# Performance work log

Hardware: AMD Instinct MI355X
Metric: run time of the kernel (lower is better)

The kernel has to match this reference:

```python
import jax, jax.numpy as jnp
import numpy as np

N_NODES = 100000
N_EDGES = 1600000
D = 128          # in_dim == out_dim
H = 8            # num_heads
DH = D // H      # head dim = 16
DFF = 2 * D
EPS_LN = 1e-5


def _ln(x, g, b):
    mu = jnp.mean(x, axis=-1, keepdims=True)
    var = jnp.var(x, axis=-1, keepdims=True)
    return (x - mu) * jax.lax.rsqrt(var + EPS_LN) * g + b


def setup_inputs() -> dict:
    key = jax.random.key(0)
    ks = jax.random.split(key, 12)
    s = 1.0 / np.sqrt(D)
    inp = {
        "h": jax.random.normal(ks[0], (N_NODES, D), jnp.float32),
        "src": jax.random.randint(ks[1], (N_EDGES,), 0, N_NODES, jnp.int32),
        "dst": jax.random.randint(ks[2], (N_EDGES,), 0, N_NODES, jnp.int32),
        "Wq": jax.random.normal(ks[3], (D, D), jnp.float32) * s,
        "Wk": jax.random.normal(ks[4], (D, D), jnp.float32) * s,
        "Wv": jax.random.normal(ks[5], (D, D), jnp.float32) * s,
        "Wo": jax.random.normal(ks[6], (D, D), jnp.float32) * s,
        "bo": jnp.zeros((D,), jnp.float32),
        "ln1_g": jnp.ones((D,), jnp.float32),
        "ln1_b": jnp.zeros((D,), jnp.float32),
        "W1": jax.random.normal(ks[7], (D, DFF), jnp.float32) * s,
        "b1": jnp.zeros((DFF,), jnp.float32),
        "W2": jax.random.normal(ks[8], (DFF, D), jnp.float32) * (1.0 / np.sqrt(DFF)),
        "b2": jnp.zeros((D,), jnp.float32),
        "ln2_g": jnp.ones((D,), jnp.float32),
        "ln2_b": jnp.zeros((D,), jnp.float32),
    }
    return inp


def reference(h, src, dst, Wq, Wk, Wv, Wo, bo, ln1_g, ln1_b, W1, b1, W2, b2, ln2_g, ln2_b):
    n = h.shape[0]
    # Q/K/V projections (no bias), split into heads: [N, H, DH]
    Q = (h @ Wq).reshape(n, H, DH)
    K = (h @ Wk).reshape(n, H, DH)
    V = (h @ Wv).reshape(n, H, DH)

    # edge-wise attention score: K[src] . Q[dst] / sqrt(DH), exp-clamped
    score = jnp.einsum("ehd,ehd->eh", K[src], Q[dst]) / np.sqrt(DH)  # [E, H]
    score = jnp.exp(jnp.clip(score, -5.0, 5.0))

    # weighted message sum + normalizer via segment reduce over dst
    m = V[src] * score[:, :, None]                                   # [E, H, DH]
    wV = jax.ops.segment_sum(m, dst, num_segments=n)                 # [N, H, DH]
    z = jax.ops.segment_sum(score, dst, num_segments=n)              # [N, H]

    h_attn = (wV / (z[:, :, None] + 1e-6)).reshape(n, D)

    # output projection + residual + LN
    x = h + (h_attn @ Wo + bo)
    x = _ln(x, ln1_g, ln1_b)

    # FFN + residual + LN
    y = jax.nn.relu(x @ W1 + b1) @ W2 + b2
    x = _ln(x + y, ln2_g, ln2_b)
    return x
```

## Files before the change

### kernel.cpp

```cpp
#include <hip/hip_runtime.h>
#include <hip/hip_bf16.h>
#include <math.h>


typedef __attribute__((ext_vector_type(8))) short bf16x8;
typedef __attribute__((ext_vector_type(4))) float f32x4;
typedef __attribute__((ext_vector_type(2))) _Float16 half2_t;

#define BSHIFT 9
#define BSIZE  512

static __device__ __forceinline__ half2_t h2(unsigned u) {
    return __builtin_bit_cast(half2_t, u);
}
static __device__ __forceinline__ float bl(unsigned u) {
    return __uint_as_float(u << 16);
}
static __device__ __forceinline__ float bh(unsigned u) {
    return __uint_as_float(u & 0xffff0000u);
}

template<int K, bool AF32, bool RELU, bool LN, bool RESID, bool BIAS, bool YW, bool F16O>
__global__ __launch_bounds__(256)
void gemm_mfma(const void* __restrict__ Ap, int lda,
               const __hip_bfloat16* __restrict__ Bt, int ldbt,
               const float* __restrict__ bias, const float* __restrict__ resid,
               const float* __restrict__ lng, const float* __restrict__ lnb,
               float* __restrict__ Cf, __hip_bfloat16* __restrict__ Cb, int ldc,
               size_t bt_ystride, size_t cb_ystride, int N)
{
    constexpr int CK = 128;
    __shared__ unsigned short As[64 * 136];
    __shared__ unsigned short Bs[128 * 136];

    const int tid  = threadIdx.x;
    const int row0 = blockIdx.x * 64;
    int col0 = 0;
    if (YW) { Bt += blockIdx.y * bt_ystride; Cb += blockIdx.y * cb_ystride; }
    else    col0 = blockIdx.y * 128;

    const int wave = tid >> 6, lane = tid & 63;
    const int quad = lane >> 4, l15 = lane & 15;

    f32x4 acc[8];
    #pragma unroll
    for (int t = 0; t < 8; ++t) acc[t] = (f32x4)0.f;

    for (int kc = 0; kc < K; kc += CK) {
        #pragma unroll
        for (int it = 0; it < 4; ++it) {
            int i = tid + it * 256;
            int r = i >> 4, kb = i & 15;
            int rg = row0 + r; if (rg > N - 1) rg = N - 1;
            if (AF32) {
                const float* Af = (const float*)Ap;
                const float4 f0 = *(const float4*)&Af[(size_t)rg * lda + kc + kb * 8];
                const float4 f1 = *(const float4*)&Af[(size_t)rg * lda + kc + kb * 8 + 4];
                __hip_bfloat162 b01 = __float22bfloat162_rn(make_float2(f0.x, f0.y));
                __hip_bfloat162 b23 = __float22bfloat162_rn(make_float2(f0.z, f0.w));
                __hip_bfloat162 b45 = __float22bfloat162_rn(make_float2(f1.x, f1.y));
                __hip_bfloat162 b67 = __float22bfloat162_rn(make_float2(f1.z, f1.w));
                uint4 u;
                u.x = *(unsigned*)&b01; u.y = *(unsigned*)&b23;
                u.z = *(unsigned*)&b45; u.w = *(unsigned*)&b67;
                *(uint4*)&As[r * 136 + kb * 8] = u;
            } else {
                const __hip_bfloat16* Ab = (const __hip_bfloat16*)Ap;
                *(uint4*)&As[r * 136 + kb * 8] =
                    *(const uint4*)&Ab[(size_t)rg * lda + kc + kb * 8];
            }
        }
        #pragma unroll
        for (int it = 0; it < 8; ++it) {
            int i = tid + it * 256;
            int r = i >> 4, kb = i & 15;
            *(uint4*)&Bs[r * 136 + kb * 8] =
                *(const uint4*)&Bt[(size_t)(col0 + r) * ldbt + kc + kb * 8];
        }
        __syncthreads();
        const unsigned short* ap = &As[(wave * 16 + l15) * 136 + quad * 8];
        const unsigned short* bp = &Bs[l15 * 136 + quad * 8];
        #pragma unroll
        for (int ks = 0; ks < 4; ++ks) {
            bf16x8 a = *(const bf16x8*)(ap + ks * 32);
            #pragma unroll
            for (int t = 0; t < 8; ++t) {
                bf16x8 b = *(const bf16x8*)(bp + t * 16 * 136 + ks * 32);
                acc[t] = __builtin_amdgcn_mfma_f32_16x16x32_bf16(a, b, acc[t], 0, 0, 0);
            }
        }
        __syncthreads();
    }

    const int rbase = row0 + wave * 16 + quad * 4;

    float vals[8][4];
    #pragma unroll
    for (int t = 0; t < 8; ++t) {
        float bv = BIAS ? bias[col0 + t * 16 + l15] : 0.f;
        #pragma unroll
        for (int i = 0; i < 4; ++i) vals[t][i] = acc[t][i] + bv;
    }
    if (RESID) {
        #pragma unroll
        for (int i = 0; i < 4; ++i) {
            int row = rbase + i;
            if (row < N) {
                #pragma unroll
                for (int t = 0; t < 8; ++t)
                    vals[t][i] += resid[(size_t)row * 128 + t * 16 + l15];
            }
        }
    }
    if (RELU) {
        #pragma unroll
        for (int t = 0; t < 8; ++t)
            #pragma unroll
            for (int i = 0; i < 4; ++i) vals[t][i] = fmaxf(vals[t][i], 0.f);
    }
    if (LN) {
        #pragma unroll
        for (int i = 0; i < 4; ++i) {
            float s = 0.f, sq = 0.f;
            #pragma unroll
            for (int t = 0; t < 8; ++t) { float v = vals[t][i]; s += v; sq += v * v; }
            s  += __shfl_xor(s, 1);  s  += __shfl_xor(s, 2);
            s  += __shfl_xor(s, 4);  s  += __shfl_xor(s, 8);
            sq += __shfl_xor(sq, 1); sq += __shfl_xor(sq, 2);
            sq += __shfl_xor(sq, 4); sq += __shfl_xor(sq, 8);
            float m  = s * (1.f / 128.f);
            float rs = rsqrtf(sq * (1.f / 128.f) - m * m + 1e-5f);
            #pragma unroll
            for (int t = 0; t < 8; ++t) {
                float g = lng[t * 16 + l15], b = lnb[t * 16 + l15];
                vals[t][i] = (vals[t][i] - m) * rs * g + b;
            }
        }
    }
    #pragma unroll
    for (int i = 0; i < 4; ++i) {
        int row = rbase + i;
        if (row >= N) continue;
        if (Cf) {
            #pragma unroll
            for (int t = 0; t < 8; ++t)
                Cf[(size_t)row * ldc + col0 + t * 16 + l15] = vals[t][i];
        }
        if (Cb) {
            #pragma unroll
            for (int t = 0; t < 8; ++t) {
                if (F16O)
                    ((_Float16*)Cb)[(size_t)row * ldc + col0 + t * 16 + l15] =
                        (_Float16)vals[t][i];
                else
                    Cb[(size_t)row * ldc + col0 + t * 16 + l15] =
                        __float2bfloat16(vals[t][i]);
            }
        }
    }
}

struct WArgs {
    const float* src[6];
    __hip_bfloat16* dst[6];
    int R[6], C[6];
};
__global__ __launch_bounds__(256)
void cast_w(WArgs wa)
{
    int w = blockIdx.y;
    int R = wa.R[w], C = wa.C[w];
    int i = blockIdx.x * 256 + threadIdx.x;
    if (i >= R * C) return;
    int sh = (C == 256) ? 8 : 7;
    int r = i >> sh, c = i & (C - 1);
    wa.dst[w][(size_t)c * R + r] = __float2bfloat16(wa.src[w][i]);
}

__global__ __launch_bounds__(256)
void bucket_hist(const int* __restrict__ dst, int* __restrict__ bCnt,
                 int E, int chunk, int NB)
{
    __shared__ int bh[256];
    const int t = threadIdx.x;
    bh[t] = 0;
    __syncthreads();
    const int s0 = blockIdx.x * chunk;
    const int s1 = min(E, s0 + chunk);
    for (int i = s0 + t; i < s1; i += 256)
        atomicAdd(&bh[dst[i] >> BSHIFT], 1);
    __syncthreads();
    if (t < NB && bh[t]) atomicAdd(&bCnt[t], bh[t]);
}

__global__ __launch_bounds__(256)
void bucket_scan(const int* __restrict__ bCnt, int* __restrict__ bBase,
                 int* __restrict__ gCur, int* __restrict__ rowStart,
                 int N, int E, int NB)
{
    __shared__ int wsum[4];
    const int t = threadIdx.x, lane = t & 63, wv = t >> 6;
    int v = (t < NB) ? bCnt[t] : 0;
    const int s = v;
    for (int off = 1; off < 64; off <<= 1) {
        int u = __shfl_up(v, off);
        if (lane >= off) v += u;
    }
    if (lane == 63) wsum[wv] = v;
    __syncthreads();
    int add = 0;
    for (int w = 0; w < wv; ++w) add += wsum[w];
    const int excl = v + add - s;
    if (t <= NB) bBase[t] = excl;
    if (t < NB)  gCur[t]  = excl;
    if (t == 0)  rowStart[N] = E;
}

__global__ __launch_bounds__(256)
void partition_kernel(const int* __restrict__ src, const int* __restrict__ dst,
                      int* __restrict__ gCur, uint2* __restrict__ P,
                      int E, int chunk, int NB)
{
    __shared__ int ch[256];
    __shared__ int cur[256];
    const int t = threadIdx.x;
    ch[t] = 0;
    __syncthreads();
    const int s0 = blockIdx.x * chunk;
    const int s1 = min(E, s0 + chunk);
    for (int i = s0 + t; i < s1; i += 256)
        atomicAdd(&ch[dst[i] >> BSHIFT], 1);
    __syncthreads();
    if (t < NB) {
        int c = ch[t];
        cur[t] = c ? atomicAdd(&gCur[t], c) : 0;
    }
    __syncthreads();
    for (int i = s0 + t; i < s1; i += 256) {
        int d = dst[i];
        int pos = atomicAdd(&cur[d >> BSHIFT], 1);
        P[pos] = make_uint2((unsigned)src[i], (unsigned)d);
    }
}

__global__ __launch_bounds__(256)
void bucket_scatter(const uint2* __restrict__ P, const int* __restrict__ bBase,
                    int* __restrict__ rowStart, int* __restrict__ esrc, int N)
{
    __shared__ int hist[BSIZE];
    __shared__ int cur[BSIZE];
    __shared__ int wsum[4];

    const int b  = blockIdx.x;
    const int t  = threadIdx.x;
    const int d0 = b << BSHIFT;
    const int bb  = bBase[b];
    const int cnt = bBase[b + 1] - bb;

    hist[t] = 0; hist[t + 256] = 0;
    __syncthreads();
    for (int i = t; i < cnt; i += 256)
        atomicAdd(&hist[(int)P[bb + i].y - d0], 1);
    __syncthreads();

    {
        const int a0 = hist[2 * t], a1 = hist[2 * t + 1];
        int v = a0 + a1;
        const int s = v;
        const int lane = t & 63, wv = t >> 6;
        for (int off = 1; off < 64; off <<= 1) {
            int u = __shfl_up(v, off);
            if (lane >= off) v += u;
        }
        if (lane == 63) wsum[wv] = v;
        __syncthreads();
        int add = 0;
        for (int w = 0; w < wv; ++w) add += wsum[w];
        const int exclT = v + add - s;
        cur[2 * t]     = exclT;
        cur[2 * t + 1] = exclT + a0;
    }
    __syncthreads();
    for (int i = t; i < BSIZE; i += 256) {
        int d = d0 + i;
        if (d < N) rowStart[d] = bb + cur[i];
    }
    __syncthreads();
    for (int i = t; i < cnt; i += 256) {
        uint2 p = P[bb + i];
        int pos = atomicAdd(&cur[(int)p.y - d0], 1);
        esrc[bb + pos] = (int)p.x;
    }
}

__global__ __launch_bounds__(256)
void aggregate_kernel(unsigned short* __restrict__ Qp,
                      const unsigned short* __restrict__ KV,
                      const int* __restrict__ esrc,
                      const int* __restrict__ rowStart, int N)
{
    const int lane = threadIdx.x & 63;
    const int wid  = threadIdx.x >> 6;
    const int d    = blockIdx.x * 4 + wid;
    if (d >= N) return;

    const int c = lane & 15;
    const int g = lane >> 4;

    const uint4 qraw = *(const uint4*)(Qp + (size_t)d * 128u + c * 8);
    const half2_t q0 = h2(qraw.x), q1 = h2(qraw.y),
                  q2 = h2(qraw.z), q3 = h2(qraw.w);

    const int beg = rowStart[d];
    const int end = rowStart[d + 1];

    float a0 = 0.f, a1 = 0.f, a2 = 0.f, a3 = 0.f;
    float a4 = 0.f, a5 = 0.f, a6 = 0.f, a7 = 0.f, z = 0.f;
    const float S = 0.36067376022224085f;
    const float C = 7.2134752044448170f;
    const char* KVb = (const char*)KV + (size_t)c * 16;

    for (int base = beg; base < end; base += 64) {
        int n = end - base; if (n > 64) n = 64;
        const int mysrc = (lane < n) ? esrc[base + lane] : 0;
        const int jmax = (n + 3) >> 2;
        #pragma unroll 2
        for (int j = 0; j < jmax; ++j) {
            const int idx = j * 4 + g;
            const bool valid = idx < n;
            const int s = __shfl(mysrc, valid ? idx : n - 1);
            const char* bp = KVb + (size_t)(unsigned)s * 512u;
            const uint4 kr = *(const uint4*)bp;
            const uint4 vr = *(const uint4*)(bp + 256);
            float p = __builtin_amdgcn_fdot2(h2(kr.x), q0, 0.f, false);
            p = __builtin_amdgcn_fdot2(h2(kr.y), q1, p, false);
            p = __builtin_amdgcn_fdot2(h2(kr.z), q2, p, false);
            p = __builtin_amdgcn_fdot2(h2(kr.w), q3, p, false);
            p += __shfl_xor(p, 1);
            float se = exp2f(fminf(C, fmaxf(-C, p * S)));
            se = valid ? se : 0.f;
            a0 += bl(vr.x) * se; a1 += bh(vr.x) * se;
            a2 += bl(vr.y) * se; a3 += bh(vr.y) * se;
            a4 += bl(vr.z) * se; a5 += bh(vr.z) * se;
            a6 += bl(vr.w) * se; a7 += bh(vr.w) * se;
            z  += se;
        }
    }

    a0 += __shfl_xor(a0, 16); a1 += __shfl_xor(a1, 16);
    a2 += __shfl_xor(a2, 16); a3 += __shfl_xor(a3, 16);
    a4 += __shfl_xor(a4, 16); a5 += __shfl_xor(a5, 16);
    a6 += __shfl_xor(a6, 16); a7 += __shfl_xor(a7, 16);
    z  += __shfl_xor(z, 16);
    a0 += __shfl_xor(a0, 32); a1 += __shfl_xor(a1, 32);
    a2 += __shfl_xor(a2, 32); a3 += __shfl_xor(a3, 32);
    a4 += __shfl_xor(a4, 32); a5 += __shfl_xor(a5, 32);
    a6 += __shfl_xor(a6, 32); a7 += __shfl_xor(a7, 32);
    z  += __shfl_xor(z, 32);

    if (g == 0) {
        const float inv = 1.0f / (z + 1e-6f);
        __hip_bfloat162 p0 = __float22bfloat162_rn(make_float2(a0 * inv, a1 * inv));
        __hip_bfloat162 p1 = __float22bfloat162_rn(make_float2(a2 * inv, a3 * inv));
        __hip_bfloat162 p2 = __float22bfloat162_rn(make_float2(a4 * inv, a5 * inv));
        __hip_bfloat162 p3 = __float22bfloat162_rn(make_float2(a6 * inv, a7 * inv));
        uint4 o;
        o.x = *(unsigned*)&p0; o.y = *(unsigned*)&p1;
        o.z = *(unsigned*)&p2; o.w = *(unsigned*)&p3;
        *(uint4*)(Qp + (size_t)d * 128u + c * 8) = o;
    }
}

extern "C" void kernel_launch(void* const* d_in, const int* in_sizes, int n_in,
                              void* d_out, int out_size, void* d_ws, size_t ws_size,
                              hipStream_t stream)
{
    const float* h    = (const float*)d_in[0];
    const int*   src  = (const int*)  d_in[1];
    const int*   dst  = (const int*)  d_in[2];
    const float* Wq   = (const float*)d_in[3];
    const float* Wk   = (const float*)d_in[4];
    const float* Wv   = (const float*)d_in[5];
    const float* Wo   = (const float*)d_in[6];
    const float* bo   = (const float*)d_in[7];
    const float* ln1g = (const float*)d_in[8];
    const float* ln1b = (const float*)d_in[9];
    const float* W1   = (const float*)d_in[10];
    const float* b1   = (const float*)d_in[11];
    const float* W2   = (const float*)d_in[12];
    const float* b2   = (const float*)d_in[13];
    const float* ln2g = (const float*)d_in[14];
    const float* ln2b = (const float*)d_in[15];

    const int N = in_sizes[0] / 128;
    const int E = in_sizes[1];
    const int NB = (N + BSIZE - 1) >> BSHIFT;

    unsigned short* Qh = (unsigned short*)d_ws;
    unsigned short* KV = Qh + (size_t)N * 128;
    __hip_bfloat16* Xh = (__hip_bfloat16*)(KV + (size_t)N * 256);
    float*          Xf = (float*)(Xh + (size_t)N * 128);
    __hip_bfloat16* Wt = (__hip_bfloat16*)(Xf + (size_t)N * 128);
    __hip_bfloat16* Wqt = Wt;
    __hip_bfloat16* Wkt = Wqt + 16384;
    __hip_bfloat16* Wvt = Wkt + 16384;
    __hip_bfloat16* Wot = Wvt + 16384;
    __hip_bfloat16* W1t = Wot + 16384;
    __hip_bfloat16* W2t = W1t + 32768;
    int* ib       = (int*)(W2t + 32768);
    int* bCnt     = ib;
    int* bBase    = ib + 256;
    int* gCur     = ib + 514;
    int* rowStart = ib + 770;
    int* esrc     = ib + 770 + N + 2;
    uint2* P      = (uint2*)Xf;
    __hip_bfloat16* Th = (__hip_bfloat16*)KV;

    const dim3 blk(256);
    const int  nb    = (N + 63) / 64;
    const int  chunk = (E + 255) / 256;

    WArgs wa;
    wa.src[0] = Wq; wa.src[1] = Wk; wa.src[2] = Wv; wa.src[3] = Wo; wa.src[4] = W1; wa.src[5] = W2;
    wa.dst[0] = Wqt; wa.dst[1] = Wkt; wa.dst[2] = Wvt; wa.dst[3] = Wot; wa.dst[4] = W1t; wa.dst[5] = W2t;
    wa.R[0] = wa.R[1] = wa.R[2] = wa.R[3] = 128; wa.R[4] = 128; wa.R[5] = 256;
    wa.C[0] = wa.C[1] = wa.C[2] = wa.C[3] = 128; wa.C[4] = 256; wa.C[5] = 128;
    cast_w<<<dim3(128, 6), blk, 0, stream>>>(wa);

    gemm_mfma<128,true,false,false,false,false,false,true><<<dim3(nb, 1), blk, 0, stream>>>(
        h, 128, Wqt, 128, nullptr, nullptr, nullptr, nullptr,
        nullptr, (__hip_bfloat16*)Qh, 128, 0, 0, N);
    gemm_mfma<128,true,false,false,false,false,false,true><<<dim3(nb, 1), blk, 0, stream>>>(
        h, 128, Wkt, 128, nullptr, nullptr, nullptr, nullptr,
        nullptr, (__hip_bfloat16*)KV, 256, 0, 0, N);
    gemm_mfma<128,true,false,false,false,false,false,false><<<dim3(nb, 1), blk, 0, stream>>>(
        h, 128, Wvt, 128, nullptr, nullptr, nullptr, nullptr,
        nullptr, (__hip_bfloat16*)(KV + 128), 256, 0, 0, N);

    hipMemsetAsync(bCnt, 0, 256 * sizeof(int), stream);
    bucket_hist<<<dim3(256), blk, 0, stream>>>(dst, bCnt, E, chunk, NB);
    bucket_scan<<<dim3(1), blk, 0, stream>>>(bCnt, bBase, gCur, rowStart, N, E, NB);
    partition_kernel<<<dim3(256), blk, 0, stream>>>(src, dst, gCur, P, E, chunk, NB);
    bucket_scatter<<<dim3(NB), blk, 0, stream>>>(P, bBase, rowStart, esrc, N);

    aggregate_kernel<<<dim3((N + 3) / 4), blk, 0, stream>>>(Qh, KV, esrc, rowStart, N);

    gemm_mfma<128,false,false,true,true,true,false,false><<<dim3(nb, 1), blk, 0, stream>>>(
        (__hip_bfloat16*)Qh, 128, Wot, 128, bo, h, ln1g, ln1b, Xf, Xh, 128, 0, 0, N);

    gemm_mfma<128,false,true,false,false,true,false,false><<<dim3(nb, 2), blk, 0, stream>>>(
        Xh, 128, W1t, 128, b1, nullptr, nullptr, nullptr, nullptr, Th, 256, 0, 0, N);

    gemm_mfma<256,false,false,true,true,true,false,false><<<dim3(nb, 1), blk, 0, stream>>>(
        Th, 256, W2t, 256, b2, Xf, ln2g, ln2b, (float*)d_out, nullptr, 128, 0, 0, N);
}
```

Measured before the change: 431.8 us.

## Fuse Q/K/V projections into one kernel and loop W1 column halves in-block

Replaces three separate Q, K and V GEMM launches with one kernel that converts each 64-row tile of h to bf16 once and reuses it for all three weight matrices. The W1 GEMM now loops over both 128-column halves inside a block instead of using a 2-wide grid, so the A tile is loaded once. The bucket counter memset is folded into the weight-cast kernel. The aim is to cut repeated reads of h and Xh and to remove launch overhead. In exchange, each block does more serial work with fewer blocks in flight.

Result: faster. 419.9 us (-2.8%).

```diff
diff --git a/kernel.cpp b/kernel.cpp
--- a/kernel.cpp
+++ b/kernel.cpp
@@ -20,139 +20,205 @@
     return __uint_as_float(u & 0xffff0000u);
 }
 
-template<int K, bool AF32, bool RELU, bool LN, bool RESID, bool BIAS, bool YW, bool F16O>
-__global__ __launch_bounds__(256)
-void gemm_mfma(const void* __restrict__ Ap, int lda,
+__global__ __launch_bounds__(256)
+void qkv_fused(const float* __restrict__ h,
+               const __hip_bfloat16* __restrict__ Wqt,
+               const __hip_bfloat16* __restrict__ Wkt,
+               const __hip_bfloat16* __restrict__ Wvt,
+               unsigned short* __restrict__ Qh,
+               unsigned short* __restrict__ KV,
+               int N)
+{
+    __shared__ unsigned short As[64 * 136];
+    __shared__ unsigned short Bs[128 * 136];
+
+    const int tid  = threadIdx.x;
+    const int row0 = blockIdx.x * 64;
+    const int wave = tid >> 6, lane = tid & 63;
+    const int quad = lane >> 4, l15 = lane & 15;
+
+    #pragma unroll
+    for (int it = 0; it < 4; ++it) {
+        int i = tid + it * 256;
+        int r = i >> 4, kb = i & 15;
+        int rg = row0 + r; if (rg > N - 1) rg = N - 1;
+        const float4 f0 = *(const float4*)&h[(size_t)rg * 128 + kb * 8];
+        const float4 f1 = *(const float4*)&h[(size_t)rg * 128 + kb * 8 + 4];
+        __hip_bfloat162 b01 = __float22bfloat162_rn(make_float2(f0.x, f0.y));
+        __hip_bfloat162 b23 = __float22bfloat162_rn(make_float2(f0.z, f0.w));
+        __hip_bfloat162 b45 = __float22bfloat162_rn(make_float2(f1.x, f1.y));
+        __hip_bfloat162 b67 = __float22bfloat162_rn(make_float2(f1.z, f1.w));
+        uint4 u;
+        u.x = *(unsigned*)&b01; u.y = *(unsigned*)&b23;
+        u.z = *(unsigned*)&b45; u.w = *(unsigned*)&b67;
+        *(uint4*)&As[r * 136 + kb * 8] = u;
+    }
+
+    const __hip_bfloat16* Ws[3] = { Wqt, Wkt, Wvt };
+
+    #pragma unroll
+    for (int w = 0; w < 3; ++w) {
+        #pragma unroll
+        for (int it = 0; it < 8; ++it) {
+            int i = tid + it * 256;
+            int r = i >> 4, kb = i & 15;
+            *(uint4*)&Bs[r * 136 + kb * 8] =
+                *(const uint4*)&Ws[w][(size_t)r * 128 + kb * 8];
+        }
+        __syncthreads();
+
+        f32x4 acc[8];
+        #pragma unroll
+        for (int t = 0; t < 8; ++t) acc[t] = (f32x4)0.f;
+
+        const unsigned short* ap = &As[(wave * 16 + l15) * 136 + quad * 8];
+        const unsigned short* bp = &Bs[l15 * 136 + quad * 8];
+        #pragma unroll
+        for (int ks = 0; ks < 4; ++ks) {
+            bf16x8 a = *(const bf16x8*)(ap + ks * 32);
+            #pragma unroll
+            for (int t = 0; t < 8; ++t) {
+                bf16x8 b = *(const bf16x8*)(bp + t * 16 * 136 + ks * 32);
+                acc[t] = __builtin_amdgcn_mfma_f32_16x16x32_bf16(a, b, acc[t], 0, 0, 0);
+            }
+        }
+        __syncthreads();
+
+        const int rbase = row0 + wave * 16 + quad * 4;
+        #pragma unroll
+        for (int i = 0; i < 4; ++i) {
+            int row = rbase + i;
+            if (row >= N) continue;
+            #pragma unroll
+            for (int t = 0; t < 8; ++t) {
+                float v = acc[t][i];
+                if (w == 0)
+                    ((_Float16*)Qh)[(size_t)row * 128 + t * 16 + l15] = (_Float16)v;
+                else if (w == 1)
+                    ((_Float16*)KV)[(size_t)row * 256 + t * 16 + l15] = (_Float16)v;
+                else
+                    ((__hip_bfloat16*)KV)[(size_t)row * 256 + 128 + t * 16 + l15] =
+                        __float2bfloat16(v);
+            }
+        }
+    }
+}
+
+template<int K, int YLOOP, bool RELU, bool LN, bool RESID, bool BIAS>
+__global__ __launch_bounds__(256)
+void gemm_mfma(const __hip_bfloat16* __restrict__ Ab, int lda,
                const __hip_bfloat16* __restrict__ Bt, int ldbt,
                const float* __restrict__ bias, const float* __restrict__ resid,
                const float* __restrict__ lng, const float* __restrict__ lnb,
                float* __restrict__ Cf, __hip_bfloat16* __restrict__ Cb, int ldc,
-               size_t bt_ystride, size_t cb_ystride, int N)
+               int N)
 {
     constexpr int CK = 128;
+    static_assert(YLOOP == 1 || K == CK, "YLOOP>1 needs single K chunk");
     __shared__ unsigned short As[64 * 136];
     __shared__ unsigned short Bs[128 * 136];
 
     const int tid  = threadIdx.x;
     const int row0 = blockIdx.x * 64;
-    int col0 = 0;
-    if (YW) { Bt += blockIdx.y * bt_ystride; Cb += blockIdx.y * cb_ystride; }
-    else    col0 = blockIdx.y * 128;
-
     const int wave = tid >> 6, lane = tid & 63;
     const int quad = lane >> 4, l15 = lane & 15;
-
-    f32x4 acc[8];
-    #pragma unroll
-    for (int t = 0; t < 8; ++t) acc[t] = (f32x4)0.f;
-
-    for (int kc = 0; kc < K; kc += CK) {
-        #pragma unroll
-        for (int it = 0; it < 4; ++it) {
-            int i = tid + it * 256;
-            int r = i >> 4, kb = i & 15;
-            int rg = row0 + r; if (rg > N - 1) rg = N - 1;
-            if (AF32) {
-                const float* Af = (const float*)Ap;
-                const float4 f0 = *(const float4*)&Af[(size_t)rg * lda + kc + kb * 8];
-                const float4 f1 = *(const float4*)&Af[(size_t)rg * lda + kc + kb * 8 + 4];
-                __hip_bfloat162 b01 = __float22bfloat162_rn(make_float2(f0.x, f0.y));
-                __hip_bfloat162 b23 = __float22bfloat162_rn(make_float2(f0.z, f0.w));
-                __hip_bfloat162 b45 = __float22bfloat162_rn(make_float2(f1.x, f1.y));
-                __hip_bfloat162 b67 = __float22bfloat162_rn(make_float2(f1.z, f1.w));
-                uint4 u;
-                u.x = *(unsigned*)&b01; u.y = *(unsigned*)&b23;
-                u.z = *(unsigned*)&b45; u.w = *(unsigned*)&b67;
-                *(uint4*)&As[r * 136 + kb * 8] = u;
-            } else {
-                const __hip_bfloat16* Ab = (const __hip_bfloat16*)Ap;
-                *(uint4*)&As[r * 136 + kb * 8] =
-                    *(const uint4*)&Ab[(size_t)rg * lda + kc + kb * 8];
-            }
-        }
-        #pragma unroll
-        for (int it = 0; it < 8; ++it) {
-            int i = tid + it * 256;
-            int r = i >> 4, kb = i & 15;
-            *(uint4*)&Bs[r * 136 + kb * 8] =
-                *(const uint4*)&Bt[(size_t)(col0 + r) * ldbt + kc + kb * 8];
-        }
-        __syncthreads();
-        const unsigned short* ap = &As[(wave * 16 + l15) * 136 + quad * 8];
-        const unsigned short* bp = &Bs[l15 * 136 + quad * 8];
-        #pragma unroll
-        for (int ks = 0; ks < 4; ++ks) {
-            bf16x8 a = *(const bf16x8*)(ap + ks * 32);
-            #pragma unroll
-            for (int t = 0; t < 8; ++t) {
-                bf16x8 b = *(const bf16x8*)(bp + t * 16 * 136 + ks * 32);
-                acc[t] = __builtin_amdgcn_mfma_f32_16x16x32_bf16(a, b, acc[t], 0, 0, 0);
-            }
-        }
-        __syncthreads();
-    }
-
     const int rbase = row0 + wave * 16 + quad * 4;
 
-    float vals[8][4];
-    #pragma unroll
-    for (int t = 0; t < 8; ++t) {
-        float bv = BIAS ? bias[col0 + t * 16 + l15] : 0.f;
-        #pragma unroll
-        for (int i = 0; i < 4; ++i) vals[t][i] = acc[t][i] + bv;
-    }
-    if (RESID) {
+    for (int yy = 0; yy < YLOOP; ++yy) {
+        const int col0 = yy * 128;
+
+        f32x4 acc[8];
+        #pragma unroll
+        for (int t = 0; t < 8; ++t) acc[t] = (f32x4)0.f;
+
+        for (int kc = 0; kc < K; kc += CK) {
+            if (yy == 0) {
+                #pragma unroll
+                for (int it = 0; it < 4; ++it) {
+                    int i = tid + it * 256;
+                    int r = i >> 4, kb = i & 15;
+                    int rg = row0 + r; if (rg > N - 1) rg = N - 1;
+                    *(uint4*)&As[r * 136 + kb * 8] =
+                        *(const uint4*)&Ab[(size_t)rg * lda + kc + kb * 8];
+                }
+            }
+            #pragma unroll
+            for (int it = 0; it < 8; ++it) {
+                int i = tid + it * 256;
+                int r = i >> 4, kb = i & 15;
+                *(uint4*)&Bs[r * 136 + kb * 8] =
+                    *(const uint4*)&Bt[(size_t)(col0 + r) * ldbt + kc + kb * 8];
+            }
+            __syncthreads();
+            const unsigned short* ap = &As[(wave * 16 + l15) * 136 + quad * 8];
+            const unsigned short* bp = &Bs[l15 * 136 + quad * 8];
+            #pragma unroll
+            for (int ks = 0; ks < 4; ++ks) {
+                bf16x8 a = *(const bf16x8*)(ap + ks * 32);
+                #pragma unroll
+                for (int t = 0; t < 8; ++t) {
+                    bf16x8 b = *(const bf16x8*)(bp + t * 16 * 136 + ks * 32);
+                    acc[t] = __builtin_amdgcn_mfma_f32_16x16x32_bf16(a, b, acc[t], 0, 0, 0);
+                }
+            }
+            __syncthreads();
+        }
+
+        float vals[8][4];
+        #pragma unroll
+        for (int t = 0; t < 8; ++t) {
+            float bv = BIAS ? bias[col0 + t * 16 + l15] : 0.f;
+            #pragma unroll
+            for (int i = 0; i < 4; ++i) vals[t][i] = acc[t][i] + bv;
+        }
+        if (RESID) {
+            #pragma unroll
+            for (int i = 0; i < 4; ++i) {
+                int row = rbase + i;
+                if (row < N) {
+                    #pragma unroll
+                    for (int t = 0; t < 8; ++t)
+                        vals[t][i] += resid[(size_t)row * 128 + t * 16 + l15];
+                }
+            }
+        }
+        if (RELU) {
+            #pragma unroll
+            for (int t = 0; t < 8; ++t)
+                #pragma unroll
+                for (int i = 0; i < 4; ++i) vals[t][i] = fmaxf(vals[t][i], 0.f);
+        }
+        if (LN) {
+            #pragma unroll
+            for (int i = 0; i < 4; ++i) {
+                float s = 0.f, sq = 0.f;
+                #pragma unroll
+                for (int t = 0; t < 8; ++t) { float v = vals[t][i]; s += v; sq += v * v; }
+                s  += __shfl_xor(s, 1);  s  += __shfl_xor(s, 2);
+                s  += __shfl_xor(s, 4);  s  += __shfl_xor(s, 8);
+                sq += __shfl_xor(sq, 1); sq += __shfl_xor(sq, 2);
+                sq += __shfl_xor(sq, 4); sq += __shfl_xor(sq, 8);
+                float m  = s * (1.f / 128.f);
+                float rs = rsqrtf(sq * (1.f / 128.f) - m * m + 1e-5f);
+                #pragma unroll
+                for (int t = 0; t < 8; ++t) {
+                    float g = lng[t * 16 + l15], b = lnb[t * 16 + l15];
+                    vals[t][i] = (vals[t][i] - m) * rs * g + b;
+                }
+            }
+        }
         #pragma unroll
         for (int i = 0; i < 4; ++i) {
             int row = rbase + i;
-            if (row < N) {
+            if (row >= N) continue;
+            if (Cf) {
                 #pragma unroll
                 for (int t = 0; t < 8; ++t)
-                    vals[t][i] += resid[(size_t)row * 128 + t * 16 + l15];
-            }
-        }
-    }
-    if (RELU) {
-        #pragma unroll
-        for (int t = 0; t < 8; ++t)
-            #pragma unroll
-            for (int i = 0; i < 4; ++i) vals[t][i] = fmaxf(vals[t][i], 0.f);
-    }
-    if (LN) {
-        #pragma unroll
-        for (int i = 0; i < 4; ++i) {
-            float s = 0.f, sq = 0.f;
-            #pragma unroll
-            for (int t = 0; t < 8; ++t) { float v = vals[t][i]; s += v; sq += v * v; }
-            s  += __shfl_xor(s, 1);  s  += __shfl_xor(s, 2);
-            s  += __shfl_xor(s, 4);  s  += __shfl_xor(s, 8);
-            sq += __shfl_xor(sq, 1); sq += __shfl_xor(sq, 2);
-            sq += __shfl_xor(sq, 4); sq += __shfl_xor(sq, 8);
-            float m  = s * (1.f / 128.f);
-            float rs = rsqrtf(sq * (1.f / 128.f) - m * m + 1e-5f);
-            #pragma unroll
-            for (int t = 0; t < 8; ++t) {
-                float g = lng[t * 16 + l15], b = lnb[t * 16 + l15];
-                vals[t][i] = (vals[t][i] - m) * rs * g + b;
-            }
-        }
-    }
-    #pragma unroll
-    for (int i = 0; i < 4; ++i) {
-        int row = rbase + i;
-        if (row >= N) continue;
-        if (Cf) {
-            #pragma unroll
-            for (int t = 0; t < 8; ++t)
-                Cf[(size_t)row * ldc + col0 + t * 16 + l15] = vals[t][i];
-        }
-        if (Cb) {
-            #pragma unroll
-            for (int t = 0; t < 8; ++t) {
-                if (F16O)
-                    ((_Float16*)Cb)[(size_t)row * ldc + col0 + t * 16 + l15] =
-                        (_Float16)vals[t][i];
-                else
+                    Cf[(size_t)row * ldc + col0 + t * 16 + l15] = vals[t][i];
+            }
+            if (Cb) {
+                #pragma unroll
+                for (int t = 0; t < 8; ++t)
                     Cb[(size_t)row * ldc + col0 + t * 16 + l15] =
                         __float2bfloat16(vals[t][i]);
             }
@@ -166,8 +232,9 @@
     int R[6], C[6];
 };
 __global__ __launch_bounds__(256)
-void cast_w(WArgs wa)
-{
+void cast_w(WArgs wa, int* __restrict__ bCnt)
+{
+    if (blockIdx.x == 0 && blockIdx.y == 0) bCnt[threadIdx.x] = 0;
     int w = blockIdx.y;
     int R = wa.R[w], C = wa.C[w];
     int i = blockIdx.x * 256 + threadIdx.x;
@@ -425,19 +492,10 @@
     wa.dst[0] = Wqt; wa.dst[1] = Wkt; wa.dst[2] = Wvt; wa.dst[3] = Wot; wa.dst[4] = W1t; wa.dst[5] = W2t;
     wa.R[0] = wa.R[1] = wa.R[2] = wa.R[3] = 128; wa.R[4] = 128; wa.R[5] = 256;
     wa.C[0] = wa.C[1] = wa.C[2] = wa.C[3] = 128; wa.C[4] = 256; wa.C[5] = 128;
-    cast_w<<<dim3(128, 6), blk, 0, stream>>>(wa);
-
-    gemm_mfma<128,true,false,false,false,false,false,true><<<dim3(nb, 1), blk, 0, stream>>>(
-        h, 128, Wqt, 128, nullptr, nullptr, nullptr, nullptr,
-        nullptr, (__hip_bfloat16*)Qh, 128, 0, 0, N);
-    gemm_mfma<128,true,false,false,false,false,false,true><<<dim3(nb, 1), blk, 0, stream>>>(
-        h, 128, Wkt, 128, nullptr, nullptr, nullptr, nullptr,
-        nullptr, (__hip_bfloat16*)KV, 256, 0, 0, N);
-    gemm_mfma<128,true,false,false,false,false,false,false><<<dim3(nb, 1), blk, 0, stream>>>(
-        h, 128, Wvt, 128, nullptr, nullptr, nullptr, nullptr,
-        nullptr, (__hip_bfloat16*)(KV + 128), 256, 0, 0, N);
-
-    hipMemsetAsync(bCnt, 0, 256 * sizeof(int), stream);
+    cast_w<<<dim3(128, 6), blk, 0, stream>>>(wa, bCnt);
+
+    qkv_fused<<<dim3(nb), blk, 0, stream>>>(h, Wqt, Wkt, Wvt, Qh, KV, N);
+
     bucket_hist<<<dim3(256), blk, 0, stream>>>(dst, bCnt, E, chunk, NB);
     bucket_scan<<<dim3(1), blk, 0, stream>>>(bCnt, bBase, gCur, rowStart, N, E, NB);
     partition_kernel<<<dim3(256), blk, 0, stream>>>(src, dst, gCur, P, E, chunk, NB);
@@ -445,12 +503,12 @@
 
     aggregate_kernel<<<dim3((N + 3) / 4), blk, 0, stream>>>(Qh, KV, esrc, rowStart, N);
 
-    gemm_mfma<128,false,false,true,true,true,false,false><<<dim3(nb, 1), blk, 0, stream>>>(
-        (__hip_bfloat16*)Qh, 128, Wot, 128, bo, h, ln1g, ln1b, Xf, Xh, 128, 0, 0, N);
-
-    gemm_mfma<128,false,true,false,false,true,false,false><<<dim3(nb, 2), blk, 0, stream>>>(
-        Xh, 128, W1t, 128, b1, nullptr, nullptr, nullptr, nullptr, Th, 256, 0, 0, N);
-
-    gemm_mfma<256,false,false,true,true,true,false,false><<<dim3(nb, 1), blk, 0, stream>>>(
-        Th, 256, W2t, 256, b2, Xf, ln2g, ln2b, (float*)d_out, nullptr, 128, 0, 0, N);
-}
+    gemm_mfma<128,1,false,true,true,true><<<dim3(nb), blk, 0, stream>>>(
+        (const __hip_bfloat16*)Qh, 128, Wot, 128, bo, h, ln1g, ln1b, Xf, Xh, 128, N);
+
+    gemm_mfma<128,2,true,false,false,true><<<dim3(nb), blk, 0, stream>>>(
+        Xh, 128, W1t, 128, b1, nullptr, nullptr, nullptr, nullptr, Th, 256, N);
+
+    gemm_mfma<256,1,false,true,true,true><<<dim3(nb), blk, 0, stream>>>(
+        Th, 256, W2t, 256, b2, Xf, ln2g, ln2b, (float*)d_out, nullptr, 128, N);
+}
```
